# Performance work log

Hardware: AMD Instinct MI355X
Metric: run time of the kernel (lower is better)

The kernel has to match this reference:

```python
import jax, jax.numpy as jnp
import numpy as np

NUM_AGES = 100
FEAT_DIM = 512
BATCH = 4096
TEMPERATURE = 0.1
EPS = 1e-6


def setup_inputs() -> dict:
    key = jax.random.key(0)
    k1, k2, k3 = jax.random.split(key, 3)
    z_age = jax.random.normal(k1, (BATCH, FEAT_DIM), dtype=jnp.float32)
    ages = jax.random.randint(k2, (BATCH,), 0, NUM_AGES, dtype=jnp.int64)
    proxies = jax.random.normal(k3, (NUM_AGES, FEAT_DIM), dtype=jnp.float32)
    return {"z_age": z_age, "ages": ages, "proxies": proxies}


def _unit_diff(a, b):
    d = a - b
    return d / (jnp.linalg.norm(d, axis=-1, keepdims=True) + EPS)


def reference(z_age, ages, proxies):
    # Vectorized equivalent of the O(B^2) python double loop.
    # Only pairs with age_i < age_j contribute (age_i > age_j branch is a no-op `...`).
    B = z_age.shape[0]
    A = proxies.shape[0]
    aj = ages.astype(jnp.int32)
    c_cur = proxies[aj]                                   # [B, D]
    c_next = proxies[jnp.minimum(aj + 1, A - 1)]          # [B, D]
    c_prev = proxies[jnp.maximum(aj - 1, 0)]              # [B, D]
    vf = _unit_diff(c_next, c_cur)                        # forward direction per sample j
    vb = _unit_diff(c_prev, c_cur)                        # backward direction per sample j

    # Pairwise norms via Gram matrix: ||z_i - z_j||.
    G = z_age @ z_age.T                                   # [B, B]
    sq = jnp.diagonal(G)                                  # [B]
    d2 = jnp.maximum(sq[:, None] + sq[None, :] - 2.0 * G, 0.0)
    norm = jnp.sqrt(d2)                                   # [B, B]
    denom = norm + EPS

    # dot(v_d_ij, v_f_j) = (z_i . vf_j - z_j . vf_j) / (||z_i - z_j|| + eps)
    Gf = z_age @ vf.T                                     # [B, B], Gf[i, j] = z_i . vf_j
    Gb = z_age @ vb.T
    dot_f = (Gf - jnp.diagonal(Gf)[None, :]) / denom
    dot_b = (Gb - jnp.diagonal(Gb)[None, :]) / denom

    # -log(exp(df/T) / (exp(df/T) + exp(db/T))) = softplus((db - df)/T)
    per_pair = jax.nn.softplus((dot_b - dot_f) / TEMPERATURE)  # [B, B]
    mask = ages[:, None] < ages[None, :]
    loss = jnp.sum(jnp.where(mask, per_pair, 0.0))
    return loss / (B * (B - 1))
```

## Files before the change

kernel.cpp:

```cpp
#include <hip/hip_runtime.h>
#include <hip/hip_bf16.h>

#define NUM_AGES 100
#define FEAT 512
#define BATCH 4096
#define EPSF 1e-6f
#define INV_T 10.0f
#define INV_NORM (1.0f / ((float)BATCH * (float)(BATCH - 1)))

#define BM 128
#define BN 64
#define BK 64
#define NTILES 1056

typedef __bf16 bf16_t;
typedef __bf16 v8bf __attribute__((ext_vector_type(8)));
typedef float v4f __attribute__((ext_vector_type(4)));

__device__ __forceinline__ void async16(const void* g, void* l) {
  __builtin_amdgcn_global_load_lds(
      (const __attribute__((address_space(1))) void*)g,
      (__attribute__((address_space(3))) void*)l, 16, 0, 0);
}

__global__ __launch_bounds__(256) void prep_kernel(
    const float* __restrict__ z, const int* __restrict__ ages,
    const float* __restrict__ proxies,
    bf16_t* __restrict__ zb, bf16_t* __restrict__ wb,
    float* __restrict__ sq, float* __restrict__ hd,
    int* __restrict__ ages_s, float* __restrict__ out)
{
  int j = blockIdx.x;
  int t = threadIdx.x;
  if (j == 0 && t == 0) out[0] = 0.0f;

  int araw = ages[j];
  int a = araw < 0 ? 0 : (araw > NUM_AGES - 1 ? NUM_AGES - 1 : araw);
  const float* cc = proxies + (size_t)a * FEAT;
  const float* cn = proxies + (size_t)(a + 1 > NUM_AGES - 1 ? NUM_AGES - 1 : a + 1) * FEAT;
  const float* cp = proxies + (size_t)(a - 1 < 0 ? 0 : a - 1) * FEAT;
  const float* zr = z + (size_t)j * FEAT;

  int cnt = 0;
#pragma unroll
  for (int e = 0; e < BATCH / 256; ++e) {
    int k = t + e * 256;
    int ak = ages[k];
    cnt += (ak < araw || (ak == araw && k < j)) ? 1 : 0;
  }

  int c0 = 2 * t;
  float2 cc2 = *(const float2*)(cc + c0);
  float2 cn2 = *(const float2*)(cn + c0);
  float2 cp2 = *(const float2*)(cp + c0);
  float2 z2  = *(const float2*)(zr + c0);
  float df0 = cn2.x - cc2.x, df1 = cn2.y - cc2.y;
  float db0 = cp2.x - cc2.x, db1 = cp2.y - cc2.y;
  float s_ff = df0 * df0 + df1 * df1;
  float s_bb = db0 * db0 + db1 * db1;
  float s_zz = z2.x * z2.x + z2.y * z2.y;
  float s_zf = z2.x * df0 + z2.y * df1;
  float s_zb = z2.x * db0 + z2.y * db1;

  float fcnt = (float)cnt;
#pragma unroll
  for (int off = 32; off > 0; off >>= 1) {
    s_ff += __shfl_down(s_ff, off, 64);
    s_bb += __shfl_down(s_bb, off, 64);
    s_zz += __shfl_down(s_zz, off, 64);
    s_zf += __shfl_down(s_zf, off, 64);
    s_zb += __shfl_down(s_zb, off, 64);
    fcnt += __shfl_down(fcnt, off, 64);
  }
  __shared__ float red[4][6];
  int wv = t >> 6, lane = t & 63;
  if (lane == 0) {
    red[wv][0] = s_ff; red[wv][1] = s_bb; red[wv][2] = s_zz;
    red[wv][3] = s_zf; red[wv][4] = s_zb; red[wv][5] = fcnt;
  }
  __syncthreads();
  float ff = red[0][0] + red[1][0] + red[2][0] + red[3][0];
  float bb = red[0][1] + red[1][1] + red[2][1] + red[3][1];
  float zz = red[0][2] + red[1][2] + red[2][2] + red[3][2];
  float zdf = red[0][3] + red[1][3] + red[2][3] + red[3][3];
  float zdb = red[0][4] + red[1][4] + red[2][4] + red[3][4];
  int rank = (int)(red[0][5] + red[1][5] + red[2][5] + red[3][5]);

  float rf = 1.0f / (sqrtf(ff) + EPSF);
  float rb = 1.0f / (sqrtf(bb) + EPSF);
  int key = rank & 7;
  int c2s = (c0 & ~63) | (((((c0 >> 3) & 7) ^ key) << 3)) | (c0 & 7);
  float w0 = db0 * rb - df0 * rf;
  float w1 = db1 * rb - df1 * rf;
  union { bf16_t h[2]; unsigned u; } uz, uw;
  uz.h[0] = (bf16_t)z2.x; uz.h[1] = (bf16_t)z2.y;
  uw.h[0] = (bf16_t)w0;   uw.h[1] = (bf16_t)w1;
  *(unsigned*)((char*)zb + ((size_t)rank * FEAT + c2s) * 2) = uz.u;
  *(unsigned*)((char*)wb + ((size_t)rank * FEAT + c2s) * 2) = uw.u;
  if (t == 0) {
    sq[rank] = zz;
    hd[rank] = rb * zdb - rf * zdf;
    ages_s[rank] = araw;
  }
}

__global__ __launch_bounds__(256, 4) void pair_kernel(
    const bf16_t* __restrict__ zb, const bf16_t* __restrict__ wb,
    const float* __restrict__ sq, const float* __restrict__ hd,
    const int* __restrict__ ages, float* __restrict__ out)
{
  __shared__ __attribute__((aligned(16))) char lds[32768];
  __shared__ float s_sqi[BM];
  __shared__ int   s_agei[BM];
  __shared__ float s_sqj[BN];
  __shared__ float s_hdj[BN];
  __shared__ int   s_agej[BN];
  __shared__ float wsum[4];

  int t = threadIdx.x;
  int wv = t >> 6, lane = t & 63;

  int rem = blockIdx.x;
  int by = 0;
  while (rem >= 64 - 2 * by) { rem -= 64 - 2 * by; ++by; }
  int bx = 2 * by + rem;
  int i0 = by * BM, j0 = bx * BN;

  if (t < BM) {
    s_sqi[t] = sq[i0 + t];
    s_agei[t] = ages[i0 + t];
  } else if (t < BM + BN) {
    int u = t - BM;
    s_sqj[u] = sq[j0 + u];
    s_hdj[u] = hd[j0 + u];
    s_agej[u] = ages[j0 + u];
  }

  v4f accG[4][2], accH[4][2];
#pragma unroll
  for (int a = 0; a < 4; ++a)
#pragma unroll
    for (int b = 0; b < 2; ++b) {
      accG[a][b] = (v4f){0.f, 0.f, 0.f, 0.f};
      accH[a][b] = (v4f){0.f, 0.f, 0.f, 0.f};
    }

  int wm = wv >> 1, wn = wv & 1;
  int lm = lane & 15, q = lane >> 4;
  int psw0 = ((q     ) ^ (lm & 7)) * 16;
  int psw1 = ((q + 4 ) ^ (lm & 7)) * 16;

  int loff = (lane >> 3) * FEAT + (lane & 7) * 8;
  const bf16_t* baseA = zb + (size_t)i0 * FEAT + loff;
  const bf16_t* baseZ = zb + (size_t)j0 * FEAT + loff;
  const bf16_t* baseW = wb + (size_t)j0 * FEAT + loff;

  for (int k0 = 0; k0 < FEAT; k0 += BK) {
#pragma unroll
    for (int c = 0; c < 4; ++c) {
      int chunk = wv * 4 + c;
      async16(baseA + (size_t)chunk * 8 * FEAT + k0, lds + chunk * 1024);
    }
#pragma unroll
    for (int c = 0; c < 2; ++c) {
      int chunk = wv * 2 + c;
      async16(baseZ + (size_t)chunk * 8 * FEAT + k0, lds + 16384 + chunk * 1024);
      async16(baseW + (size_t)chunk * 8 * FEAT + k0, lds + 24576 + chunk * 1024);
    }
    __syncthreads();

#pragma unroll
    for (int s = 0; s < 2; ++s) {
      int psw = s ? psw1 : psw0;
      v8bf afr[4], bz[2], bw[2];
#pragma unroll
      for (int mi = 0; mi < 4; ++mi) {
        int r = wm * 64 + mi * 16 + lm;
        afr[mi] = *(const v8bf*)(lds + r * 128 + psw);
      }
#pragma unroll
      for (int ni = 0; ni < 2; ++ni) {
        int r = wn * 32 + ni * 16 + lm;
        bz[ni] = *(const v8bf*)(lds + 16384 + r * 128 + psw);
        bw[ni] = *(const v8bf*)(lds + 24576 + r * 128 + psw);
      }
#pragma unroll
      for (int mi = 0; mi < 4; ++mi)
#pragma unroll
        for (int ni = 0; ni < 2; ++ni) {
          accG[mi][ni] = __builtin_amdgcn_mfma_f32_16x16x32_bf16(afr[mi], bz[ni], accG[mi][ni], 0, 0, 0);
          accH[mi][ni] = __builtin_amdgcn_mfma_f32_16x16x32_bf16(afr[mi], bw[ni], accH[mi][ni], 0, 0, 0);
        }
    }
    __syncthreads();
  }

  float tsum = 0.f;
#pragma unroll
  for (int ni = 0; ni < 2; ++ni) {
    int jl = wn * 32 + ni * 16 + lm;
    float sqj = s_sqj[jl];
    float hdj = s_hdj[jl];
    int aj = s_agej[jl];
#pragma unroll
    for (int mi = 0; mi < 4; ++mi) {
#pragma unroll
      for (int r = 0; r < 4; ++r) {
        int il = wm * 64 + mi * 16 + q * 4 + r;
        float g = accG[mi][ni][r];
        float h = accH[mi][ni][r];
        float d2 = fmaxf(s_sqi[il] + sqj - 2.0f * g, 1e-12f);
        float rs = __builtin_amdgcn_rsqf(d2);
        float arg = (h - hdj) * INV_T * rs;
        float sp = fmaxf(arg, 0.0f) + __logf(1.0f + __expf(-fabsf(arg)));
        tsum += (s_agei[il] < aj) ? sp : 0.0f;
      }
    }
  }

#pragma unroll
  for (int off = 32; off > 0; off >>= 1) tsum += __shfl_down(tsum, off, 64);
  if (lane == 0) wsum[wv] = tsum;
  __syncthreads();
  if (t == 0)
    atomicAdd(out, (wsum[0] + wsum[1] + wsum[2] + wsum[3]) * INV_NORM);
}

extern "C" void kernel_launch(void* const* d_in, const int* in_sizes, int n_in,
                              void* d_out, int out_size, void* d_ws, size_t ws_size,
                              hipStream_t stream) {
  const float* z = (const float*)d_in[0];
  const int* ages = (const int*)d_in[1];
  const float* proxies = (const float*)d_in[2];
  float* out = (float*)d_out;

  char* ws = (char*)d_ws;
  bf16_t* zb = (bf16_t*)ws;
  bf16_t* wb = (bf16_t*)(ws + (size_t)4 * 1024 * 1024);
  size_t o = (size_t)8 * 1024 * 1024;
  float* sq      = (float*)(ws + o);
  float* hd      = (float*)(ws + o + 16384);
  int*   ages_s  = (int*)  (ws + o + 32768);

  prep_kernel<<<BATCH, 256, 0, stream>>>(z, ages, proxies, zb, wb, sq, hd, ages_s, out);
  pair_kernel<<<NTILES, 256, 0, stream>>>(zb, wb, sq, hd, ages_s, out);
}
```

Measured before the change: 102.0 us.

## Double-buffer LDS tiles and remap tile order into XCD-grouped super-blocks

Adds a second LDS buffer so the global-to-LDS loads of the next K slice are issued before the MFMA work on the current slice. This removes one barrier per iteration and hides load latency. The block-to-tile mapping is also rewritten to group 8x8 super-tiles per XCD chunk, for better L2 reuse of the zb/wb rows. In exchange, LDS use doubles to 64KB, which lowers occupancy (launch bounds drop from 4 to 2 blocks). The mapping loop also adds scalar index arithmetic at kernel start.

After: 112.1 us. 1.1x slower.

```diff
diff --git a/kernel.cpp b/kernel.cpp
--- a/kernel.cpp
+++ b/kernel.cpp
@@ -12,6 +12,8 @@
 #define BN 64
 #define BK 64
 #define NTILES 1056
+#define NXCD 8
+#define CHUNK (NTILES / NXCD)
 
 typedef __bf16 bf16_t;
 typedef __bf16 v8bf __attribute__((ext_vector_type(8)));
@@ -104,12 +106,12 @@
   }
 }
 
-__global__ __launch_bounds__(256, 4) void pair_kernel(
+__global__ __launch_bounds__(256, 2) void pair_kernel(
     const bf16_t* __restrict__ zb, const bf16_t* __restrict__ wb,
     const float* __restrict__ sq, const float* __restrict__ hd,
     const int* __restrict__ ages, float* __restrict__ out)
 {
-  __shared__ __attribute__((aligned(16))) char lds[32768];
+  __shared__ __attribute__((aligned(16))) char lds[2][32768];
   __shared__ float s_sqi[BM];
   __shared__ int   s_agei[BM];
   __shared__ float s_sqj[BN];
@@ -120,10 +122,33 @@
   int t = threadIdx.x;
   int wv = t >> 6, lane = t & 63;
 
-  int rem = blockIdx.x;
-  int by = 0;
-  while (rem >= 64 - 2 * by) { rem -= 64 - 2 * by; ++by; }
-  int bx = 2 * by + rem;
+  int by = 0, bx = 0;
+  {
+    int rem = (blockIdx.x & 7) * CHUNK + (blockIdx.x >> 3);
+    int done = 0;
+    for (int sy = 0; sy < 4 && !done; ++sy) {
+      for (int sx = 0; sx < 8 && !done; ++sx) {
+        int cnt = 0;
+        for (int r = 0; r < 8; ++r) {
+          int b = 8 * sy + r;
+          int lo = 2 * b; if (lo < 8 * sx) lo = 8 * sx;
+          int ww = 8 * sx + 8 - lo; if (ww < 0) ww = 0;
+          cnt += ww;
+        }
+        if (rem < cnt) {
+          for (int r = 0; r < 8 && !done; ++r) {
+            int b = 8 * sy + r;
+            int lo = 2 * b; if (lo < 8 * sx) lo = 8 * sx;
+            int ww = 8 * sx + 8 - lo; if (ww < 0) ww = 0;
+            if (rem < ww) { by = b; bx = lo + rem; done = 1; }
+            else rem -= ww;
+          }
+        } else {
+          rem -= cnt;
+        }
+      }
+    }
+  }
   int i0 = by * BM, j0 = bx * BN;
 
   if (t < BM) {
@@ -155,20 +180,38 @@
   const bf16_t* baseZ = zb + (size_t)j0 * FEAT + loff;
   const bf16_t* baseW = wb + (size_t)j0 * FEAT + loff;
 
-  for (int k0 = 0; k0 < FEAT; k0 += BK) {
-#pragma unroll
-    for (int c = 0; c < 4; ++c) {
-      int chunk = wv * 4 + c;
-      async16(baseA + (size_t)chunk * 8 * FEAT + k0, lds + chunk * 1024);
-    }
-#pragma unroll
-    for (int c = 0; c < 2; ++c) {
-      int chunk = wv * 2 + c;
-      async16(baseZ + (size_t)chunk * 8 * FEAT + k0, lds + 16384 + chunk * 1024);
-      async16(baseW + (size_t)chunk * 8 * FEAT + k0, lds + 24576 + chunk * 1024);
-    }
-    __syncthreads();
-
+#pragma unroll
+  for (int c = 0; c < 4; ++c) {
+    int chunk = wv * 4 + c;
+    async16(baseA + (size_t)chunk * 8 * FEAT, lds[0] + chunk * 1024);
+  }
+#pragma unroll
+  for (int c = 0; c < 2; ++c) {
+    int chunk = wv * 2 + c;
+    async16(baseZ + (size_t)chunk * 8 * FEAT, lds[0] + 16384 + chunk * 1024);
+    async16(baseW + (size_t)chunk * 8 * FEAT, lds[0] + 24576 + chunk * 1024);
+  }
+  __syncthreads();
+
+  int cur = 0;
+  for (int it = 0; it < FEAT / BK; ++it) {
+    if (it + 1 < FEAT / BK) {
+      int k0n = (it + 1) * BK;
+      char* nb = lds[cur ^ 1];
+#pragma unroll
+      for (int c = 0; c < 4; ++c) {
+        int chunk = wv * 4 + c;
+        async16(baseA + (size_t)chunk * 8 * FEAT + k0n, nb + chunk * 1024);
+      }
+#pragma unroll
+      for (int c = 0; c < 2; ++c) {
+        int chunk = wv * 2 + c;
+        async16(baseZ + (size_t)chunk * 8 * FEAT + k0n, nb + 16384 + chunk * 1024);
+        async16(baseW + (size_t)chunk * 8 * FEAT + k0n, nb + 24576 + chunk * 1024);
+      }
+    }
+
+    const char* cb = lds[cur];
 #pragma unroll
     for (int s = 0; s < 2; ++s) {
       int psw = s ? psw1 : psw0;
@@ -176,13 +219,13 @@
 #pragma unroll
       for (int mi = 0; mi < 4; ++mi) {
         int r = wm * 64 + mi * 16 + lm;
-        afr[mi] = *(const v8bf*)(lds + r * 128 + psw);
+        afr[mi] = *(const v8bf*)(cb + r * 128 + psw);
       }
 #pragma unroll
       for (int ni = 0; ni < 2; ++ni) {
         int r = wn * 32 + ni * 16 + lm;
-        bz[ni] = *(const v8bf*)(lds + 16384 + r * 128 + psw);
-        bw[ni] = *(const v8bf*)(lds + 24576 + r * 128 + psw);
+        bz[ni] = *(const v8bf*)(cb + 16384 + r * 128 + psw);
+        bw[ni] = *(const v8bf*)(cb + 24576 + r * 128 + psw);
       }
 #pragma unroll
       for (int mi = 0; mi < 4; ++mi)
@@ -192,7 +235,11 @@
           accH[mi][ni] = __builtin_amdgcn_mfma_f32_16x16x32_bf16(afr[mi], bw[ni], accH[mi][ni], 0, 0, 0);
         }
     }
-    __syncthreads();
+
+    if (it + 1 < FEAT / BK) {
+      __syncthreads();
+      cur ^= 1;
+    }
   }
 
   float tsum = 0.f;
```
